# Kernel optimization log

Hardware: AMD Instinct MI355X
Metric: run time of the kernel (lower is better)

## Reference

```python
import jax, jax.numpy as jnp
import numpy as np

EMB = 768  # SentenceT5 embedding dim; MLP input is 2*EMB


def setup_inputs() -> dict:
    key = jax.random.key(0)
    ks = jax.random.split(key, 9)
    B, S, D = 32, 32, 64
    num_doc = jax.random.randint(ks[0], (B,), 8, D + 1, dtype=jnp.int32)
    num_doc = num_doc.at[0].set(D)  # ensure max == padded dim (tf.reduce_max semantics)
    num_seg = jax.random.randint(ks[1], (B,), 4, S + 1, dtype=jnp.int32)
    num_seg = num_seg.at[0].set(S)
    doc_emb = jax.random.normal(ks[2], (B, D, EMB), jnp.float32)
    sum_emb = jax.random.normal(ks[3], (B, S, EMB), jnp.float32)
    # ragged .to_tensor() -> zero rows beyond per-sample length
    doc_emb = doc_emb * (jnp.arange(D)[None, :, None] < num_doc[:, None, None])
    sum_emb = sum_emb * (jnp.arange(S)[None, :, None] < num_seg[:, None, None])
    target_agg = jax.random.uniform(ks[4], (B,), jnp.float32)
    target_inst = jax.random.uniform(ks[5], (B, S), jnp.float32)
    w = lambda k, i, o: jax.random.normal(k, (i, o), jnp.float32) * 0.02
    W1 = w(ks[6], 2 * EMB, EMB)
    b1 = jnp.zeros((EMB,), jnp.float32)
    W2 = w(ks[7], EMB, EMB // 2)
    b2 = jnp.zeros((EMB // 2,), jnp.float32)
    W3 = w(ks[8], EMB // 2, 1)
    b3 = jnp.zeros((1,), jnp.float32)
    return dict(doc_emb=doc_emb, sum_emb=sum_emb, num_document_splits=num_doc,
                num_summary_segments=num_seg, target_agg_score=target_agg,
                target_instance_score=target_inst,
                W1=W1, b1=b1, W2=W2, b2=b2, W3=W3, b3=b3)


def _forward(doc_emb, sum_emb, num_doc, num_seg, W1, b1, W2, b2, W3, b3):
    B, D, E = doc_emb.shape
    S = sum_emb.shape[1]
    # concat([doc, seg]) @ W1 == doc @ W1[:E] + seg @ W1[E:]  (avoids materializing [B,S,D,2E])
    h_doc = jnp.einsum('bde,eh->bdh', doc_emb, W1[:E])   # [B,D,E]
    h_seg = jnp.einsum('bse,eh->bsh', sum_emb, W1[E:])   # [B,S,E]
    h1 = jax.nn.gelu(h_doc[:, None, :, :] + h_seg[:, :, None, :] + b1, approximate=False)  # [B,S,D,E]
    h2 = jax.nn.gelu(jnp.einsum('bsdh,hk->bsdk', h1, W2) + b2, approximate=False)          # [B,S,D,E/2]
    score = jax.nn.sigmoid(jnp.einsum('bsdk,ko->bsdo', h2, W3) + b3)[..., 0]               # [B,S,D]
    mask_d = (jnp.arange(D)[None, :] < num_doc[:, None]).astype(jnp.float32)               # [B,D]
    seg_max = jnp.max(mask_d[:, None, :] * score, axis=-1)                                 # [B,S]
    seg_w = jnp.where(num_seg > 10, 1.0, 100.0).astype(jnp.float32)                        # [B]
    pred = seg_w[:, None] * seg_max                                                        # [B,S]
    # cosine similarity prior (keras CosineSimilarity returns -cos)
    dn = doc_emb * jax.lax.rsqrt(jnp.maximum(jnp.sum(doc_emb * doc_emb, -1, keepdims=True), 1e-12))
    sn = sum_emb * jax.lax.rsqrt(jnp.maximum(jnp.sum(sum_emb * sum_emb, -1, keepdims=True), 1e-12))
    cs = -jnp.einsum('bde,bse->bsd', dn, sn)                                               # [B,S,D]
    dscos = jnp.max(mask_d[:, None, :] * (1.0 + cs) * 0.5, axis=-1)                        # [B,S]
    seg_mask = (jnp.arange(S)[None, :] < num_seg[:, None]).astype(jnp.float32)             # [B,S]
    diff = jnp.abs(dscos - pred) * seg_mask
    cos_prior = jnp.mean(jnp.sum(diff, axis=1) / num_seg.astype(jnp.float32))
    return pred, cos_prior


def reference(doc_emb, sum_emb, num_document_splits, num_summary_segments,
              target_agg_score, target_instance_score,
              W1, b1, W2, b2, W3, b3):
    B, S = target_instance_score.shape
    seg_mask = jnp.arange(S)[None, :] < num_summary_segments[:, None]
    # pad target instance scores with ones beyond per-sample length
    target_instance = jnp.where(seg_mask, target_instance_score, 1.0)
    pred, cos_prior = _forward(doc_emb, sum_emb, num_document_splits, num_summary_segments,
                               W1, b1, W2, b2, W3, b3)
    return (target_agg_score, target_instance, pred, num_summary_segments, cos_prior)
```

## Files before the change

### kernel.cpp

```cpp
#include <hip/hip_runtime.h>
#include <hip/hip_bf16.h>
#include <math.h>


typedef __bf16 bf16x8 __attribute__((ext_vector_type(8)));
typedef float f32x4 __attribute__((ext_vector_type(4)));

__device__ __forceinline__ unsigned short f2bf(float x) {
    unsigned int u = __float_as_uint(x);
    u = (u + 0x7fffu + ((u >> 16) & 1u)) >> 16;
    return (unsigned short)u;
}
__device__ __forceinline__ float exp2_fast(float x) {
    float r; asm("v_exp_f32 %0, %1" : "=v"(r) : "v"(x)); return r;
}
__device__ __forceinline__ float rcp_fast(float x) {
    float r; asm("v_rcp_f32 %0, %1" : "=v"(r) : "v"(x)); return r;
}
__device__ __forceinline__ unsigned int cvt_pk_bf16(float lo, float hi) {
    unsigned int r; asm("v_cvt_pk_bf16_f32 %0, %1, %2" : "=v"(r) : "v"(lo), "v"(hi)); return r;
}
__device__ __forceinline__ float gelu_fast(float x) {
    float t = x * fmaf(x * x, -0.10294325f, -2.3022081f);
    return x * rcp_fast(1.0f + exp2_fast(t));
}
__device__ __forceinline__ float sigmoid_fast(float x) {
    return rcp_fast(1.0f + exp2_fast(x * -1.4426950408889634f));
}
__device__ __forceinline__ float wave_sum(float v) {
    for (int o = 32; o; o >>= 1) v += __shfl_xor(v, o);
    return v;
}
__device__ __forceinline__ float wave_max(float v) {
    for (int o = 32; o; o >>= 1) v = fmaxf(v, __shfl_xor(v, o));
    return v;
}
__device__ __forceinline__ void soft_barrier() {
    __builtin_amdgcn_sched_barrier(0);
    asm volatile("s_waitcnt lgkmcnt(0)" ::: "memory");
    __builtin_amdgcn_s_barrier();
    __builtin_amdgcn_sched_barrier(0);
}
#define GLOAD_LDS16(GP, LP)                                                     \
    __builtin_amdgcn_global_load_lds(                                           \
        (const __attribute__((address_space(1))) unsigned int*)(GP),            \
        (__attribute__((address_space(3))) unsigned int*)(LP), 16, 0, 0)

__global__ __launch_bounds__(256) void prep_all(const float* __restrict__ W1,
                                                const float* __restrict__ W2,
                                                const float* __restrict__ doc,
                                                const float* __restrict__ sume,
                                                unsigned short* __restrict__ W1t,
                                                unsigned short* __restrict__ W2f,
                                                unsigned short* __restrict__ dnbf,
                                                unsigned short* __restrict__ snbf) {
    __shared__ __align__(16) char shbuf[49152];
    int id = blockIdx.x;
    int t = threadIdx.x;
    if (id < 288) {
        float (*tile)[65] = (float(*)[65])shbuf;
        int bx = id % 12, by = id / 12;
        int r0 = by * 64, c0 = bx * 64;
        #pragma unroll
        for (int p = 0; p < 16; ++p) {
            int r = p * 4 + (t >> 6), c = t & 63;
            tile[r][c] = W1[(r0 + r) * 768 + c0 + c];
        }
        __syncthreads();
        #pragma unroll
        for (int p = 0; p < 16; ++p) {
            int cc = p * 4 + (t >> 6), rr = t & 63;
            W1t[(c0 + cc) * 1536 + r0 + rr] = f2bf(tile[rr][cc]);
        }
    } else if (id < 300) {
        unsigned short* sh = (unsigned short*)shbuf;
        int kt = id - 288;
        #pragma unroll
        for (int p = 0; p < 96; ++p) {
            int u = p * 256 + t;
            int k = u / 384, n = u - k * 384;
            sh[u] = f2bf(W2[(kt * 64 + k) * 384 + n]);
        }
        __syncthreads();
        #pragma unroll
        for (int p = 0; p < 12; ++p) {
            int u = p * 256 + t;
            int lane = u & 63;
            int g = u >> 6;
            int ks = g / 24, fc = g - ks * 24;
            unsigned short tmp[8];
            #pragma unroll
            for (int j = 0; j < 8; ++j)
                tmp[j] = sh[(ks * 32 + (lane >> 4) * 8 + j) * 384 + fc * 16 + (lane & 15)];
            int ktks = kt * 2 + ks;
            *(uint4*)(W2f + ((ktks * 24 + fc) * 64 + lane) * 8) = *(uint4*)tmp;
        }
    } else {
        int row = (id - 300) * 4 + (t >> 6);
        int lane = t & 63;
        const float* p; unsigned short* dst;
        if (row < 2048) { p = doc + row * 768; dst = dnbf + row * 768; }
        else            { p = sume + (row - 2048) * 768; dst = snbf + (row - 2048) * 768; }
        const float* pp = p + lane * 12;
        float4 a0 = *(const float4*)(pp);
        float4 a1 = *(const float4*)(pp + 4);
        float4 a2 = *(const float4*)(pp + 8);
        float s = a0.x*a0.x + a0.y*a0.y + a0.z*a0.z + a0.w*a0.w
                + a1.x*a1.x + a1.y*a1.y + a1.z*a1.z + a1.w*a1.w
                + a2.x*a2.x + a2.y*a2.y + a2.z*a2.z + a2.w*a2.w;
        s = wave_sum(s);
        float r = rsqrtf(fmaxf(s, 1e-12f));
        unsigned short* dd = dst + lane * 12;
        dd[0]  = f2bf(a0.x * r); dd[1]  = f2bf(a0.y * r);
        dd[2]  = f2bf(a0.z * r); dd[3]  = f2bf(a0.w * r);
        dd[4]  = f2bf(a1.x * r); dd[5]  = f2bf(a1.y * r);
        dd[6]  = f2bf(a1.z * r); dd[7]  = f2bf(a1.w * r);
        dd[8]  = f2bf(a2.x * r); dd[9]  = f2bf(a2.y * r);
        dd[10] = f2bf(a2.z * r); dd[11] = f2bf(a2.w * r);
    }
}

__global__ __launch_bounds__(256) void gemm1(const float* __restrict__ doc,
                                             const float* __restrict__ sume,
                                             const unsigned short* __restrict__ W1t,
                                             const float* __restrict__ b1,
                                             unsigned short* __restrict__ hd,
                                             unsigned short* __restrict__ hs) {
    __shared__ __align__(16) unsigned short Asw[2][128 * 64];
    __shared__ __align__(16) unsigned short Bsw[2][64 * 64];
    int t = threadIdx.x;
    int row0 = blockIdx.y * 128, col0 = blockIdx.x * 64;
    bool is_doc = row0 < 2048;
    const float* A = is_doc ? (doc + row0 * 768) : (sume + (row0 - 2048) * 768);
    int kbase = is_doc ? 0 : 768;
    unsigned short* O = is_doc ? (hd + row0 * 768) : (hs + (row0 - 2048) * 768);

    int l = t & 63, w = t >> 6;
    int wr = w >> 1, wc = w & 1;
    int srow = t >> 3, sko = (t & 7) * 8;
    f32x4 acc[4][2];
    #pragma unroll
    for (int i = 0; i < 4; ++i)
        #pragma unroll
        for (int j = 0; j < 2; ++j) acc[i][j] = (f32x4)0.f;

    float4 fA0[4], fA1[4];
    bf16x8 bB[2];

#define G_LOAD(KT)                                                              \
    {                                                                           \
        _Pragma("unroll")                                                       \
        for (int p = 0; p < 4; ++p) {                                           \
            fA0[p] = *(const float4*)(A + (p * 32 + srow) * 768 + (KT) + sko);  \
            fA1[p] = *(const float4*)(A + (p * 32 + srow) * 768 + (KT) + sko + 4); \
        }                                                                       \
        _Pragma("unroll")                                                       \
        for (int p = 0; p < 2; ++p)                                             \
            bB[p] = *(const bf16x8*)(W1t + (col0 + p * 32 + srow) * 1536 + kbase + (KT) + sko); \
    }

#define G_STORE(BUF)                                                            \
    {                                                                           \
        char* AB = (char*)Asw[BUF];                                             \
        char* BB = (char*)Bsw[BUF];                                             \
        _Pragma("unroll")                                                       \
        for (int p = 0; p < 4; ++p) {                                           \
            uint4 v = make_uint4(cvt_pk_bf16(fA0[p].x, fA0[p].y),               \
                                 cvt_pk_bf16(fA0[p].z, fA0[p].w),               \
                                 cvt_pk_bf16(fA1[p].x, fA1[p].y),               \
                                 cvt_pk_bf16(fA1[p].z, fA1[p].w));              \
            int r = p * 32 + srow;                                              \
            int byte = (r * 128 + sko * 2) ^ ((r & 7) << 4);                    \
            *(uint4*)(AB + byte) = v;                                           \
        }                                                                       \
        _Pragma("unroll")                                                       \
        for (int p = 0; p < 2; ++p) {                                           \
            int r = p * 32 + srow;                                              \
            int byte = (r * 128 + sko * 2) ^ ((r & 7) << 4);                    \
            *(bf16x8*)(BB + byte) = bB[p];                                      \
        }                                                                       \
    }

    G_LOAD(0)
    G_STORE(0)
    G_LOAD(64)
    soft_barrier();

    #pragma unroll 1
    for (int i = 0; i < 12; ++i) {
        int cur = i & 1;
        const char* AR = (const char*)Asw[cur];
        const char* BR = (const char*)Bsw[cur];
        #pragma unroll
        for (int ks = 0; ks < 2; ++ks) {
            int koff = (ks * 32 + (l >> 4) * 8) * 2;
            bf16x8 af[4], bfr[2];
            #pragma unroll
            for (int fr = 0; fr < 4; ++fr) {
                int r = wr * 64 + fr * 16 + (l & 15);
                af[fr] = *(const bf16x8*)(AR + ((r * 128 + koff) ^ ((r & 7) << 4)));
            }
            #pragma unroll
            for (int fc = 0; fc < 2; ++fc) {
                int n = wc * 32 + fc * 16 + (l & 15);
                bfr[fc] = *(const bf16x8*)(BR + ((n * 128 + koff) ^ ((n & 7) << 4)));
            }
            #pragma unroll
            for (int fr = 0; fr < 4; ++fr)
                #pragma unroll
                for (int fc = 0; fc < 2; ++fc)
                    acc[fr][fc] = __builtin_amdgcn_mfma_f32_16x16x32_bf16(af[fr], bfr[fc], acc[fr][fc], 0, 0, 0);
        }
        if (i < 11) {
            G_STORE(cur ^ 1)
            if (i < 10) G_LOAD((i + 2) * 64)
        }
        soft_barrier();
    }
#undef G_LOAD
#undef G_STORE

    #pragma unroll
    for (int fr = 0; fr < 4; ++fr)
        #pragma unroll
        for (int fc = 0; fc < 2; ++fc) {
            int c = col0 + wc * 32 + fc * 16 + (l & 15);
            float badd = is_doc ? 0.0f : b1[c];
            #pragma unroll
            for (int j = 0; j < 4; ++j) {
                int r = wr * 64 + fr * 16 + (l >> 4) * 4 + j;
                O[r * 768 + c] = f2bf(acc[fr][fc][j] + badd);
            }
        }
}

__global__ __launch_bounds__(512) void score_mfma(
    const unsigned short* __restrict__ hd, const unsigned short* __restrict__ hs,
    const unsigned short* __restrict__ W2f,
    const float* __restrict__ b2, const float* __restrict__ W3,
    const float* __restrict__ b3, const int* __restrict__ ndoc,
    const int* __restrict__ nseg, const unsigned short* __restrict__ dnbf,
    const unsigned short* __restrict__ snbf, float* __restrict__ out,
    float* __restrict__ dscos)
{
    __shared__ __align__(16) char smem[65536];
    float* spart = (float*)smem;
    float* sred  = (float*)smem;

    int t = threadIdx.x;
    int l = t & 63, w = t >> 6;

    if (blockIdx.x < 32) {
        int b = (int)blockIdx.x;
        if (w < 4) {
            const unsigned short* sb = snbf + b * 32 * 768;
            const unsigned short* db = dnbf + b * 64 * 768;
            int arow = l & 15, ak = (l >> 4) * 8;
            int d0 = w * 16;
            f32x4 acc0 = (f32x4)0.f, acc1 = (f32x4)0.f;
            #pragma unroll
            for (int k = 0; k < 768; k += 32) {
                bf16x8 a0 = *(const bf16x8*)(sb + arow * 768 + k + ak);
                bf16x8 a1 = *(const bf16x8*)(sb + (16 + arow) * 768 + k + ak);
                bf16x8 bb = *(const bf16x8*)(db + (d0 + arow) * 768 + k + ak);
                acc0 = __builtin_amdgcn_mfma_f32_16x16x32_bf16(a0, bb, acc0, 0, 0, 0);
                acc1 = __builtin_amdgcn_mfma_f32_16x16x32_bf16(a1, bb, acc1, 0, 0, 0);
            }
            int nd = ndoc[b];
            int d = d0 + (l & 15);
            float v0[4], v1[4];
            #pragma unroll
            for (int j = 0; j < 4; ++j) {
                v0[j] = (d < nd) ? (1.f - acc0[j]) * 0.5f : 0.f;
                v1[j] = (d < nd) ? (1.f - acc1[j]) * 0.5f : 0.f;
            }
            #pragma unroll
            for (int o = 1; o < 16; o <<= 1) {
                #pragma unroll
                for (int j = 0; j < 4; ++j) {
                    v0[j] = fmaxf(v0[j], __shfl_xor(v0[j], o));
                    v1[j] = fmaxf(v1[j], __shfl_xor(v1[j], o));
                }
            }
            if ((l & 15) == 0) {
                int srw = (l >> 4) * 4;
                #pragma unroll
                for (int j = 0; j < 4; ++j) {
                    sred[w * 32 + srw + j] = v0[j];
                    sred[w * 32 + 16 + srw + j] = v1[j];
                }
            }
        }
        __syncthreads();
        if (t < 32)
            dscos[(int)blockIdx.x * 32 + t] = fmaxf(fmaxf(sred[t], sred[32 + t]),
                                                    fmaxf(sred[64 + t], sred[96 + t]));
        return;
    }

    int sb = (int)blockIdx.x - 32;
    int lb = (sb & 7) * 64 + (sb >> 3);
    int b = lb >> 4, sp = lb & 15;
    int s0 = sp * 2;
    int nd = ndoc[b], ns = nseg[b];
    int wr = w >> 2, wc = w & 3;

    f32x4 acc[4][6];
    #pragma unroll
    for (int i = 0; i < 4; ++i)
        #pragma unroll
        for (int j = 0; j < 6; ++j) acc[i][j] = (f32x4)0.f;

    int r = t >> 2;
    int k8 = t & 3;
    int d = r & 63, sl = r >> 6;
    const unsigned short* hdp = hd + (b * 64 + d) * 768 + k8 * 8;
    const unsigned short* hsp = hs + (b * 32 + s0 + sl) * 768 + k8 * 8;
    int abyte = (r >> 4) * 1024 + k8 * 256 + (r & 15) * 16;

    bf16x8 hd8, hs8;

#define A_LOAD(KT)                                                              \
    {                                                                           \
        hd8 = *(const bf16x8*)(hdp + (KT));                                     \
        hs8 = *(const bf16x8*)(hsp + (KT));                                     \
    }

#define B_STAGE(KC, BUF)                                                        \
    {                                                                           \
        _Pragma("unroll")                                                       \
        for (int q = 0; q < 3; ++q) {                                           \
            int fc = w * 3 + q;                                                 \
            const unsigned short* gsrc = W2f + (((KC) * 24 + fc) * 64 + l) * 8; \
            GLOAD_LDS16(gsrc, smem + 16384 + (BUF) * 24576 + fc * 1024);        \
        }                                                                       \
    }

#define A_STORE(BUF)                                                            \
    {                                                                           \
        const unsigned int* hu = (const unsigned int*)&hd8;                     \
        const unsigned int* su = (const unsigned int*)&hs8;                     \
        unsigned int au[4];                                                     \
        _Pragma("unroll")                                                       \
        for (int e = 0; e < 4; ++e) {                                           \
            float x0 = __uint_as_float(hu[e] << 16) + __uint_as_float(su[e] << 16); \
            float x1 = __uint_as_float(hu[e] & 0xffff0000u) + __uint_as_float(su[e] & 0xffff0000u); \
            au[e] = cvt_pk_bf16(gelu_fast(x0), gelu_fast(x1));                  \
        }                                                                       \
        *(uint4*)(smem + (BUF) * 8192 + abyte) = make_uint4(au[0], au[1], au[2], au[3]); \
    }

    B_STAGE(0, 0)
    A_LOAD(0)
    A_STORE(0)
    __builtin_amdgcn_sched_barrier(0);
    asm volatile("s_waitcnt vmcnt(0) lgkmcnt(0)" ::: "memory");
    __builtin_amdgcn_s_barrier();
    __builtin_amdgcn_sched_barrier(0);

    #pragma unroll 1
    for (int i = 0; i < 24; ++i) {
        int cur = i & 1;
        if (i < 23) {
            B_STAGE(i + 1, cur ^ 1)
            A_LOAD((i + 1) * 32)
        }
        const char* AR = (const char*)smem + cur * 8192;
        const char* BR = (const char*)smem + 16384 + cur * 24576;
        __builtin_amdgcn_s_setprio(1);
        bf16x8 af[4];
        #pragma unroll
        for (int fr = 0; fr < 4; ++fr)
            af[fr] = *(const bf16x8*)(AR + (wr * 4 + fr) * 1024 + l * 16);
        #pragma unroll
        for (int i2 = 0; i2 < 6; ++i2) {
            bf16x8 bq = *(const bf16x8*)(BR + (wc * 6 + i2) * 1024 + l * 16);
            #pragma unroll
            for (int fr = 0; fr < 4; ++fr)
                acc[fr][i2] = __builtin_amdgcn_mfma_f32_16x16x32_bf16(af[fr], bq, acc[fr][i2], 0, 0, 0);
        }
        __builtin_amdgcn_s_setprio(0);
        if (i < 23) A_STORE(cur ^ 1)
        __builtin_amdgcn_sched_barrier(0);
        asm volatile("s_waitcnt vmcnt(0) lgkmcnt(0)" ::: "memory");
        __builtin_amdgcn_s_barrier();
        __builtin_amdgcn_sched_barrier(0);
    }
#undef A_LOAD
#undef B_STAGE
#undef A_STORE

    float b2v[6], w3v[6];
    #pragma unroll
    for (int i2 = 0; i2 < 6; ++i2) {
        int col = wc * 96 + i2 * 16 + (l & 15);
        b2v[i2] = b2[col];
        w3v[i2] = W3[col];
    }
    __syncthreads();
    #pragma unroll
    for (int fr = 0; fr < 4; ++fr) {
        #pragma unroll
        for (int j = 0; j < 4; ++j) {
            float pr = 0.f;
            #pragma unroll
            for (int i2 = 0; i2 < 6; ++i2)
                pr += gelu_fast(acc[fr][i2][j] + b2v[i2]) * w3v[i2];
            pr += __shfl_xor(pr, 1);
            pr += __shfl_xor(pr, 2);
            pr += __shfl_xor(pr, 4);
            pr += __shfl_xor(pr, 8);
            if ((l & 15) == 0)
                spart[wc * 128 + wr * 64 + fr * 16 + (l >> 4) * 4 + j] = pr;
        }
    }
    __syncthreads();
    if (t < 128) {
        int row = t;
        float v = spart[row] + spart[128 + row] + spart[256 + row] + spart[384 + row] + b3[0];
        float sc = sigmoid_fast(v);
        int dd = row & 63, sl2 = row >> 6;
        float m = (dd < nd) ? sc : 0.f;
        m = wave_max(m);
        if ((t & 63) == 0) {
            float segw = (ns > 10) ? 1.f : 100.f;
            out[1056 + b * 32 + s0 + sl2] = segw * m;
        }
    }
}

__global__ __launch_bounds__(1024) void finish_k(const float* __restrict__ agg,
                                                 const float* __restrict__ tinst,
                                                 const int* __restrict__ nseg,
                                                 const float* __restrict__ dscos,
                                                 float* __restrict__ out) {
    __shared__ float red[16];
    int t = threadIdx.x, lane = t & 63, w = t >> 6;
    int b = t >> 5, s = t & 31;
    int ns = nseg[b];
    out[32 + t] = (s < ns) ? tinst[t] : 1.0f;
    if (t < 32) {
        out[t] = agg[t];
        out[2080 + t] = (float)nseg[t];
    }
    float pred = out[1056 + t];
    float v = (s < ns) ? fabsf(dscos[t] - pred) / (float)ns : 0.f;
    v = wave_sum(v);
    if (lane == 0) red[w] = v;
    __syncthreads();
    if (w == 0) {
        float x = (lane < 16) ? red[lane] : 0.f;
        x = wave_sum(x);
        if (lane == 0) out[2112] = x * (1.f / 32.f);
    }
}

extern "C" void kernel_launch(void* const* d_in, const int* in_sizes, int n_in,
                              void* d_out, int out_size, void* d_ws, size_t ws_size,
                              hipStream_t stream) {
    const float* doc   = (const float*)d_in[0];
    const float* sume  = (const float*)d_in[1];
    const int*   ndoc  = (const int*)d_in[2];
    const int*   nseg  = (const int*)d_in[3];
    const float* agg   = (const float*)d_in[4];
    const float* tinst = (const float*)d_in[5];
    const float* W1    = (const float*)d_in[6];
    const float* b1    = (const float*)d_in[7];
    const float* W2    = (const float*)d_in[8];
    const float* b2    = (const float*)d_in[9];
    const float* W3    = (const float*)d_in[10];
    const float* b3    = (const float*)d_in[11];
    float* out = (float*)d_out;
    char* ws = (char*)d_ws;

    unsigned short* hd   = (unsigned short*)(ws);
    unsigned short* hs   = (unsigned short*)(ws + 3145728);
    unsigned short* W1t  = (unsigned short*)(ws + 4718592);
    unsigned short* W2f  = (unsigned short*)(ws + 7077888);
    unsigned short* dnbf = (unsigned short*)(ws + 7667712);
    unsigned short* snbf = (unsigned short*)(ws + 10813440);
    float* dscos = (float*)(ws + 12386304);

    prep_all<<<1068, 256, 0, stream>>>(W1, W2, doc, sume, W1t, W2f, dnbf, snbf);
    gemm1<<<dim3(12, 24), 256, 0, stream>>>(doc, sume, W1t, b1, hd, hs);
    score_mfma<<<544, 512, 0, stream>>>(hd, hs, W2f, b2, W3, b3, ndoc, nseg,
                                        dnbf, snbf, out, dscos);
    finish_k<<<1, 1024, 0, stream>>>(agg, tinst, nseg, dscos, out);
}
```

Measured before the change: 103.3 us.

## Keep first-layer activations in fp32 and split score tiles across 16 waves

```diff
diff --git a/kernel.cpp b/kernel.cpp
--- a/kernel.cpp
+++ b/kernel.cpp
@@ -124,8 +124,8 @@
                                              const float* __restrict__ sume,
                                              const unsigned short* __restrict__ W1t,
                                              const float* __restrict__ b1,
-                                             unsigned short* __restrict__ hd,
-                                             unsigned short* __restrict__ hs) {
+                                             float* __restrict__ hd,
+                                             float* __restrict__ hs) {
     __shared__ __align__(16) unsigned short Asw[2][128 * 64];
     __shared__ __align__(16) unsigned short Bsw[2][64 * 64];
     int t = threadIdx.x;
@@ -133,7 +133,7 @@
     bool is_doc = row0 < 2048;
     const float* A = is_doc ? (doc + row0 * 768) : (sume + (row0 - 2048) * 768);
     int kbase = is_doc ? 0 : 768;
-    unsigned short* O = is_doc ? (hd + row0 * 768) : (hs + (row0 - 2048) * 768);
+    float* O = is_doc ? (hd + row0 * 768) : (hs + (row0 - 2048) * 768);
 
     int l = t & 63, w = t >> 6;
     int wr = w >> 1, wc = w & 1;
@@ -229,13 +229,13 @@
             #pragma unroll
             for (int j = 0; j < 4; ++j) {
                 int r = wr * 64 + fr * 16 + (l >> 4) * 4 + j;
-                O[r * 768 + c] = f2bf(acc[fr][fc][j] + badd);
-            }
-        }
-}
-
-__global__ __launch_bounds__(512) void score_mfma(
-    const unsigned short* __restrict__ hd, const unsigned short* __restrict__ hs,
+                O[r * 768 + c] = acc[fr][fc][j] + badd;
+            }
+        }
+}
+
+__global__ __launch_bounds__(1024) void score_mfma(
+    const float* __restrict__ hd, const float* __restrict__ hs,
     const unsigned short* __restrict__ W2f,
     const float* __restrict__ b2, const float* __restrict__ W3,
     const float* __restrict__ b3, const int* __restrict__ ndoc,
@@ -305,49 +305,47 @@
     int nd = ndoc[b], ns = nseg[b];
     int wr = w >> 2, wc = w & 3;
 
-    f32x4 acc[4][6];
+    f32x4 acc[2][6];
     #pragma unroll
-    for (int i = 0; i < 4; ++i)
+    for (int i = 0; i < 2; ++i)
         #pragma unroll
         for (int j = 0; j < 6; ++j) acc[i][j] = (f32x4)0.f;
 
-    int r = t >> 2;
-    int k8 = t & 3;
+    int r = t & 127;
+    int kq = t >> 7;
     int d = r & 63, sl = r >> 6;
-    const unsigned short* hdp = hd + (b * 64 + d) * 768 + k8 * 8;
-    const unsigned short* hsp = hs + (b * 32 + s0 + sl) * 768 + k8 * 8;
-    int abyte = (r >> 4) * 1024 + k8 * 256 + (r & 15) * 16;
-
-    bf16x8 hd8, hs8;
+    const float* hdp = hd + (b * 64 + d) * 768 + kq * 4;
+    const float* hsp = hs + (b * 32 + s0 + sl) * 768 + kq * 4;
+    int abyte = (r >> 4) * 1024 + (kq >> 1) * 256 + (r & 15) * 16 + (kq & 1) * 8;
+    abyte ^= ((r >> 4) & 3) << 4;
+
+    float4 hdv, hsv;
 
 #define A_LOAD(KT)                                                              \
     {                                                                           \
-        hd8 = *(const bf16x8*)(hdp + (KT));                                     \
-        hs8 = *(const bf16x8*)(hsp + (KT));                                     \
+        hdv = *(const float4*)(hdp + (KT));                                     \
+        hsv = *(const float4*)(hsp + (KT));                                     \
     }
 
 #define B_STAGE(KC, BUF)                                                        \
     {                                                                           \
-        _Pragma("unroll")                                                       \
-        for (int q = 0; q < 3; ++q) {                                           \
-            int fc = w * 3 + q;                                                 \
-            const unsigned short* gsrc = W2f + (((KC) * 24 + fc) * 64 + l) * 8; \
-            GLOAD_LDS16(gsrc, smem + 16384 + (BUF) * 24576 + fc * 1024);        \
+        if (w < 12) {                                                           \
+            _Pragma("unroll")                                                   \
+            for (int q = 0; q < 2; ++q) {                                       \
+                int fc = w * 2 + q;                                             \
+                const unsigned short* gsrc = W2f + (((KC) * 24 + fc) * 64 + l) * 8; \
+                GLOAD_LDS16(gsrc, smem + 16384 + (BUF) * 24576 + fc * 1024);    \
+            }                                                                   \
         }                                                                       \
     }
 
 #define A_STORE(BUF)                                                            \
     {                                                                           \
-        const unsigned int* hu = (const unsigned int*)&hd8;                     \
-        const unsigned int* su = (const unsigned int*)&hs8;                     \
-        unsigned int au[4];                                                     \
-        _Pragma("unroll")                                                       \
-        for (int e = 0; e < 4; ++e) {                                           \
-            float x0 = __uint_as_float(hu[e] << 16) + __uint_as_float(su[e] << 16); \
-            float x1 = __uint_as_float(hu[e] & 0xffff0000u) + __uint_as_float(su[e] & 0xffff0000u); \
-            au[e] = cvt_pk_bf16(gelu_fast(x0), gelu_fast(x1));                  \
-        }                                                                       \
-        *(uint4*)(smem + (BUF) * 8192 + abyte) = make_uint4(au[0], au[1], au[2], au[3]); \
+        float x0 = hdv.x + hsv.x, x1 = hdv.y + hsv.y;                           \
+        float x2 = hdv.z + hsv.z, x3 = hdv.w + hsv.w;                           \
+        unsigned int a0 = cvt_pk_bf16(gelu_fast(x0), gelu_fast(x1));            \
+        unsigned int a1 = cvt_pk_bf16(gelu_fast(x2), gelu_fast(x3));            \
+        *(uint2*)(smem + (BUF) * 8192 + abyte) = make_uint2(a0, a1);            \
     }
 
     B_STAGE(0, 0)
@@ -368,15 +366,17 @@
         const char* AR = (const char*)smem + cur * 8192;
         const char* BR = (const char*)smem + 16384 + cur * 24576;
         __builtin_amdgcn_s_setprio(1);
-        bf16x8 af[4];
-        #pragma unroll
-        for (int fr = 0; fr < 4; ++fr)
-            af[fr] = *(const bf16x8*)(AR + (wr * 4 + fr) * 1024 + l * 16);
+        bf16x8 af[2];
+        #pragma unroll
+        for (int fr = 0; fr < 2; ++fr) {
+            int seg = wr * 2 + fr;
+            af[fr] = *(const bf16x8*)(AR + ((seg * 1024 + l * 16) ^ ((seg & 3) << 4)));
+        }
         #pragma unroll
         for (int i2 = 0; i2 < 6; ++i2) {
             bf16x8 bq = *(const bf16x8*)(BR + (wc * 6 + i2) * 1024 + l * 16);
             #pragma unroll
-            for (int fr = 0; fr < 4; ++fr)
+            for (int fr = 0; fr < 2; ++fr)
                 acc[fr][i2] = __builtin_amdgcn_mfma_f32_16x16x32_bf16(af[fr], bq, acc[fr][i2], 0, 0, 0);
         }
         __builtin_amdgcn_s_setprio(0);
@@ -399,7 +399,7 @@
     }
     __syncthreads();
     #pragma unroll
-    for (int fr = 0; fr < 4; ++fr) {
+    for (int fr = 0; fr < 2; ++fr) {
         #pragma unroll
         for (int j = 0; j < 4; ++j) {
             float pr = 0.f;
@@ -411,7 +411,7 @@
             pr += __shfl_xor(pr, 4);
             pr += __shfl_xor(pr, 8);
             if ((l & 15) == 0)
-                spart[wc * 128 + wr * 64 + fr * 16 + (l >> 4) * 4 + j] = pr;
+                spart[wc * 128 + wr * 32 + fr * 16 + (l >> 4) * 4 + j] = pr;
         }
     }
     __syncthreads();
@@ -473,17 +473,17 @@
     float* out = (float*)d_out;
     char* ws = (char*)d_ws;
 
-    unsigned short* hd   = (unsigned short*)(ws);
-    unsigned short* hs   = (unsigned short*)(ws + 3145728);
-    unsigned short* W1t  = (unsigned short*)(ws + 4718592);
-    unsigned short* W2f  = (unsigned short*)(ws + 7077888);
-    unsigned short* dnbf = (unsigned short*)(ws + 7667712);
-    unsigned short* snbf = (unsigned short*)(ws + 10813440);
-    float* dscos = (float*)(ws + 12386304);
+    float* hd            = (float*)(ws);
+    float* hs            = (float*)(ws + 6291456);
+    unsigned short* W1t  = (unsigned short*)(ws + 9437184);
+    unsigned short* W2f  = (unsigned short*)(ws + 11796480);
+    unsigned short* dnbf = (unsigned short*)(ws + 12386304);
+    unsigned short* snbf = (unsigned short*)(ws + 15532032);
+    float* dscos = (float*)(ws + 17104896);
 
     prep_all<<<1068, 256, 0, stream>>>(W1, W2, doc, sume, W1t, W2f, dnbf, snbf);
     gemm1<<<dim3(12, 24), 256, 0, stream>>>(doc, sume, W1t, b1, hd, hs);
-    score_mfma<<<544, 512, 0, stream>>>(hd, hs, W2f, b2, W3, b3, ndoc, nseg,
-                                        dnbf, snbf, out, dscos);
+    score_mfma<<<544, 1024, 0, stream>>>(hd, hs, W2f, b2, W3, b3, ndoc, nseg,
+                                         dnbf, snbf, out, dscos);
     finish_k<<<1, 1024, 0, stream>>>(agg, tinst, nseg, dscos, out);
 }
```

After: 111.1 us. 1.08x slower.

## Deepen W2 staging to triple buffer, prefetch A two ahead, swizzle LDS

Applied to the files above, without the earlier changes.

```diff
diff --git a/kernel.cpp b/kernel.cpp
--- a/kernel.cpp
+++ b/kernel.cpp
@@ -243,7 +243,7 @@
     const unsigned short* __restrict__ snbf, float* __restrict__ out,
     float* __restrict__ dscos)
 {
-    __shared__ __align__(16) char smem[65536];
+    __shared__ __align__(16) char smem[90112];
     float* spart = (float*)smem;
     float* sred  = (float*)smem;
 
@@ -316,14 +316,14 @@
     int d = r & 63, sl = r >> 6;
     const unsigned short* hdp = hd + (b * 64 + d) * 768 + k8 * 8;
     const unsigned short* hsp = hs + (b * 32 + s0 + sl) * 768 + k8 * 8;
-    int abyte = (r >> 4) * 1024 + k8 * 256 + (r & 15) * 16;
-
-    bf16x8 hd8, hs8;
-
-#define A_LOAD(KT)                                                              \
-    {                                                                           \
-        hd8 = *(const bf16x8*)(hdp + (KT));                                     \
-        hs8 = *(const bf16x8*)(hsp + (KT));                                     \
+    int abyte = ((r >> 4) * 1024 + k8 * 256 + (r & 15) * 16) ^ (k8 << 4);
+
+    bf16x8 hdA, hsA, hdB, hsB;
+
+#define A_LOAD(KT, HD8, HS8)                                                    \
+    {                                                                           \
+        HD8 = *(const bf16x8*)(hdp + (KT));                                     \
+        HS8 = *(const bf16x8*)(hsp + (KT));                                     \
     }
 
 #define B_STAGE(KC, BUF)                                                        \
@@ -336,10 +336,10 @@
         }                                                                       \
     }
 
-#define A_STORE(BUF)                                                            \
-    {                                                                           \
-        const unsigned int* hu = (const unsigned int*)&hd8;                     \
-        const unsigned int* su = (const unsigned int*)&hs8;                     \
+#define A_STORE(HD8, HS8, BUF)                                                  \
+    {                                                                           \
+        const unsigned int* hu = (const unsigned int*)&HD8;                     \
+        const unsigned int* su = (const unsigned int*)&HS8;                     \
         unsigned int au[4];                                                     \
         _Pragma("unroll")                                                       \
         for (int e = 0; e < 4; ++e) {                                           \
@@ -350,45 +350,66 @@
         *(uint4*)(smem + (BUF) * 8192 + abyte) = make_uint4(au[0], au[1], au[2], au[3]); \
     }
 
+#define MFMA_PHASE(ABUF, BBUF)                                                  \
+    {                                                                           \
+        const char* AR = (const char*)smem + (ABUF) * 8192;                     \
+        const char* BR = (const char*)smem + 16384 + (BBUF) * 24576;            \
+        __builtin_amdgcn_s_setprio(1);                                          \
+        bf16x8 af[4];                                                           \
+        _Pragma("unroll")                                                       \
+        for (int fr = 0; fr < 4; ++fr)                                          \
+            af[fr] = *(const bf16x8*)(AR + (wr * 4 + fr) * 1024                 \
+                                         + ((l * 16) ^ ((l >> 4) << 4)));       \
+        _Pragma("unroll")                                                       \
+        for (int i2 = 0; i2 < 6; ++i2) {                                        \
+            bf16x8 bq = *(const bf16x8*)(BR + (wc * 6 + i2) * 1024 + l * 16);   \
+            _Pragma("unroll")                                                   \
+            for (int fr = 0; fr < 4; ++fr)                                      \
+                acc[fr][i2] = __builtin_amdgcn_mfma_f32_16x16x32_bf16(af[fr], bq, acc[fr][i2], 0, 0, 0); \
+        }                                                                       \
+        __builtin_amdgcn_s_setprio(0);                                          \
+    }
+
+#define SYNC_CNT()                                                              \
+    __builtin_amdgcn_sched_barrier(0);                                          \
+    asm volatile("s_waitcnt vmcnt(5) lgkmcnt(0)" ::: "memory");                 \
+    __builtin_amdgcn_s_barrier();                                               \
+    __builtin_amdgcn_sched_barrier(0);
+
+#define K_ITER(J, HDL, HSL, HDS, HSS)                                           \
+    {                                                                           \
+        int i_ = base + (J);                                                    \
+        if (i_ < 22) {                                                          \
+            B_STAGE(i_ + 2, ((J) + 2) % 3)                                      \
+            A_LOAD((i_ + 2) * 32, HDL, HSL)                                     \
+        }                                                                       \
+        MFMA_PHASE((J) & 1, (J) % 3)                                            \
+        if (i_ < 23) A_STORE(HDS, HSS, ((J) + 1) & 1)                           \
+        SYNC_CNT()                                                              \
+    }
+
+    A_LOAD(0, hdA, hsA)
     B_STAGE(0, 0)
-    A_LOAD(0)
-    A_STORE(0)
-    __builtin_amdgcn_sched_barrier(0);
-    asm volatile("s_waitcnt vmcnt(0) lgkmcnt(0)" ::: "memory");
-    __builtin_amdgcn_s_barrier();
-    __builtin_amdgcn_sched_barrier(0);
+    B_STAGE(1, 1)
+    A_STORE(hdA, hsA, 0)
+    A_LOAD(32, hdB, hsB)
+    SYNC_CNT()
 
     #pragma unroll 1
-    for (int i = 0; i < 24; ++i) {
-        int cur = i & 1;
-        if (i < 23) {
-            B_STAGE(i + 1, cur ^ 1)
-            A_LOAD((i + 1) * 32)
-        }
-        const char* AR = (const char*)smem + cur * 8192;
-        const char* BR = (const char*)smem + 16384 + cur * 24576;
-        __builtin_amdgcn_s_setprio(1);
-        bf16x8 af[4];
-        #pragma unroll
-        for (int fr = 0; fr < 4; ++fr)
-            af[fr] = *(const bf16x8*)(AR + (wr * 4 + fr) * 1024 + l * 16);
-        #pragma unroll
-        for (int i2 = 0; i2 < 6; ++i2) {
-            bf16x8 bq = *(const bf16x8*)(BR + (wc * 6 + i2) * 1024 + l * 16);
-            #pragma unroll
-            for (int fr = 0; fr < 4; ++fr)
-                acc[fr][i2] = __builtin_amdgcn_mfma_f32_16x16x32_bf16(af[fr], bq, acc[fr][i2], 0, 0, 0);
-        }
-        __builtin_amdgcn_s_setprio(0);
-        if (i < 23) A_STORE(cur ^ 1)
-        __builtin_amdgcn_sched_barrier(0);
-        asm volatile("s_waitcnt vmcnt(0) lgkmcnt(0)" ::: "memory");
-        __builtin_amdgcn_s_barrier();
-        __builtin_amdgcn_sched_barrier(0);
+    for (int base = 0; base < 24; base += 6) {
+        K_ITER(0, hdA, hsA, hdB, hsB)
+        K_ITER(1, hdB, hsB, hdA, hsA)
+        K_ITER(2, hdA, hsA, hdB, hsB)
+        K_ITER(3, hdB, hsB, hdA, hsA)
+        K_ITER(4, hdA, hsA, hdB, hsB)
+        K_ITER(5, hdB, hsB, hdA, hsA)
     }
 #undef A_LOAD
 #undef B_STAGE
 #undef A_STORE
+#undef MFMA_PHASE
+#undef SYNC_CNT
+#undef K_ITER
 
     float b2v[6], w3v[6];
     #pragma unroll
```

Result: faster. 99.20 us (-4.0%).
